# Optimization experiments

Hardware: AMD Instinct MI355X
Metric: run time of the kernel (lower is better)

Reference implementation:

```python
import jax, jax.numpy as jnp
import numpy as np

N_NODES = 50000
E_EDGES = 800000
NODE_DIM = 64
HID = 128


def _leaky(x):
    return jnp.where(x > 0, x, 0.2 * x)


def _gat_conv(x, W, a_src, a_dst, b, src, dst, heads, out_ch, concat):
    # x: [N, in]; W: [in, heads*out]; a_src/a_dst: [heads, out]
    N = x.shape[0]
    h = (x @ W).reshape(N, heads, out_ch)            # [N, H, C]
    s = (h * a_src[None]).sum(-1)                    # [N, H]
    d = (h * a_dst[None]).sum(-1)                    # [N, H]
    e = _leaky(s[src] + d[dst])                      # [E, H]
    m = jax.ops.segment_max(e, dst, num_segments=N)  # segment softmax (stable)
    ex = jnp.exp(e - m[dst])
    denom = jax.ops.segment_sum(ex, dst, num_segments=N)
    alpha = ex / denom[dst]                          # [E, H] (self-loops -> denom>0)
    out = jax.ops.segment_sum(h[src] * alpha[..., None], dst, num_segments=N)
    out = out.reshape(N, heads * out_ch) if concat else out.mean(axis=1)
    return out + b


def setup_inputs() -> dict:
    key = jax.random.key(0)
    ks = jax.random.split(key, 16)
    sc = 0.1
    inp = {
        "x": jax.random.normal(ks[0], (N_NODES, NODE_DIM), jnp.float32),
        "edge_index": jax.random.randint(ks[1], (2, E_EDGES), 0, N_NODES, jnp.int64),
        "fc_w": jax.random.normal(ks[2], (NODE_DIM, HID), jnp.float32) * sc,
        "fc_b": jnp.zeros((HID,), jnp.float32),
        "W1": jax.random.normal(ks[3], (HID, 2 * HID), jnp.float32) * sc,
        "asrc1": jax.random.normal(ks[4], (2, HID), jnp.float32) * sc,
        "adst1": jax.random.normal(ks[5], (2, HID), jnp.float32) * sc,
        "b1": jnp.zeros((2 * HID,), jnp.float32),
        "Wm": jax.random.normal(ks[6], (4, 2 * HID, 2 * HID), jnp.float32) * sc,
        "asrcm": jax.random.normal(ks[7], (4, 2, HID), jnp.float32) * sc,
        "adstm": jax.random.normal(ks[8], (4, 2, HID), jnp.float32) * sc,
        "bm": jnp.zeros((4, 2 * HID), jnp.float32),
        "W6": jax.random.normal(ks[9], (2 * HID, HID), jnp.float32) * sc,
        "asrc6": jax.random.normal(ks[10], (1, HID), jnp.float32) * sc,
        "adst6": jax.random.normal(ks[11], (1, HID), jnp.float32) * sc,
        "b6": jnp.zeros((HID,), jnp.float32),
    }
    return inp


def reference(x, edge_index, fc_w, fc_b, W1, asrc1, adst1, b1,
              Wm, asrcm, adstm, bm, W6, asrc6, adst6, b6):
    N = x.shape[0]
    loops = jnp.arange(N, dtype=edge_index.dtype)
    src = jnp.concatenate([edge_index[0], loops])  # add_self_loops=True (PyG default)
    dst = jnp.concatenate([edge_index[1], loops])

    out = jax.nn.relu(x @ fc_w + fc_b)
    out = _gat_conv(out, W1, asrc1, adst1, b1, src, dst, 2, HID, True)
    for i in range(4):
        out = _gat_conv(out, Wm[i], asrcm[i], adstm[i], bm[i], src, dst, 2, HID, True)
    out = _gat_conv(out, W6, asrc6, adst6, b6, src, dst, 1, HID, True)
    return out
```

## Files before the change

kernel.cpp:

```cpp
#include <hip/hip_runtime.h>
#include <cstdint>
#include <cstddef>

#define NN 50000
#define EE 800000
#define ET 850000

typedef unsigned short ushort_t;
typedef unsigned int uint_t;
using frag_ab = __attribute__((ext_vector_type(8))) short;
using f32x4   = __attribute__((ext_vector_type(4))) float;
using f32x2   = __attribute__((ext_vector_type(2))) float;

__device__ inline ushort_t f2b(float x) {
  union { float f; unsigned int u; } c; c.f = x;
  unsigned int u = c.u;
  u += 0x7fffu + ((u >> 16) & 1u);
  return (ushort_t)(u >> 16);
}
__device__ inline float b2f(uint_t u) {
  union { unsigned int u; float f; } c; c.u = u << 16;
  return c.f;
}
__device__ inline f32x2 unp2(uint_t u) {
  union { uint_t u; float f; } lo, hi;
  lo.u = u << 16; hi.u = u & 0xffff0000u;
  f32x2 r; r.x = lo.f; r.y = hi.f; return r;
}

__device__ inline void gload16(const ushort_t* g, ushort_t* l) {
  __builtin_amdgcn_global_load_lds(
      (const __attribute__((address_space(1))) unsigned int*)g,
      (__attribute__((address_space(3))) unsigned int*)l, 16, 0, 0);
}

__global__ __launch_bounds__(256) void k_count(const int* __restrict__ edge,
                                               int* __restrict__ counts) {
  int e = blockIdx.x * 256 + threadIdx.x;
  if (e >= ET) return;
  int dd = (e < EE) ? edge[EE + e] : (e - EE);
  atomicAdd(&counts[dd], 1);
}

__global__ __launch_bounds__(1024) void k_scan1(const int* __restrict__ counts,
                                                int* __restrict__ scn,
                                                int* __restrict__ bsum) {
  __shared__ int tmp[1024];
  int tid = threadIdx.x;
  int idx = blockIdx.x * 1024 + tid;
  int v = (idx < NN) ? counts[idx] : 0;
  tmp[tid] = v;
  __syncthreads();
  for (int o = 1; o < 1024; o <<= 1) {
    int u = (tid >= o) ? tmp[tid - o] : 0;
    __syncthreads();
    tmp[tid] += u;
    __syncthreads();
  }
  if (idx < NN) scn[idx] = tmp[tid] - v;
  if (tid == 1023) bsum[blockIdx.x] = tmp[1023];
}

__global__ __launch_bounds__(64) void k_scan2(const int* __restrict__ bsum,
                                              int* __restrict__ boff) {
  int l = threadIdx.x;
  const int NB = (NN + 1023) / 1024;
  int v = (l < NB) ? bsum[l] : 0;
  int own = v;
  for (int o = 1; o < 64; o <<= 1) {
    int u = __shfl_up(v, o);
    if (l >= o) v += u;
  }
  if (l < NB) boff[l] = v - own;
}

__global__ __launch_bounds__(1024) void k_scan3(const int* __restrict__ scn,
                                                const int* __restrict__ boff,
                                                int* __restrict__ row_ptr,
                                                int* __restrict__ cursor) {
  int idx = blockIdx.x * 1024 + threadIdx.x;
  if (idx < NN) {
    int v = scn[idx] + boff[blockIdx.x];
    row_ptr[idx] = v;
    cursor[idx] = v;
  }
  if (idx == 0) row_ptr[NN] = ET;
}

__global__ __launch_bounds__(256) void k_fill(const int* __restrict__ edge,
                                              int* __restrict__ cursor,
                                              int* __restrict__ col_src) {
  int e = blockIdx.x * 256 + threadIdx.x;
  if (e >= ET) return;
  int ss, dd;
  if (e < EE) { ss = edge[e]; dd = edge[EE + e]; }
  else        { ss = dd = e - EE; }
  int pos = atomicAdd(&cursor[dd], 1);
  col_src[pos] = ss;
}

__global__ __launch_bounds__(256) void k_prep_w(const float* __restrict__ fc_w,
                                                const float* __restrict__ W1,
                                                const float* __restrict__ Wm,
                                                const float* __restrict__ W6,
                                                ushort_t* __restrict__ fcWt,
                                                ushort_t* __restrict__ W1t,
                                                ushort_t* __restrict__ Wmt,
                                                ushort_t* __restrict__ W6t) {
  int i = blockIdx.x * 256 + threadIdx.x;
  if (i < 128 * 64) { int n = i >> 6, k = i & 63; fcWt[i] = f2b(fc_w[k * 128 + n]); return; }
  i -= 128 * 64;
  if (i < 256 * 128) { int n = i >> 7, k = i & 127; W1t[i] = f2b(W1[k * 256 + n]); return; }
  i -= 256 * 128;
  if (i < 4 * 256 * 256) {
    int l = i >> 16, r2 = i & 65535, n = r2 >> 8, k = r2 & 255;
    Wmt[i] = f2b(Wm[(size_t)l * 65536 + k * 256 + n]); return;
  }
  i -= 4 * 256 * 256;
  if (i < 128 * 256) { int n = i >> 8, k = i & 255; W6t[i] = f2b(W6[k * 128 + n]); return; }
}

__global__ __launch_bounds__(256) void k_gemm_f32(const float* __restrict__ A,
                                                  const ushort_t* __restrict__ Bt,
                                                  ushort_t* __restrict__ C,
                                                  int M, int K, int Nc,
                                                  const float* __restrict__ bias) {
  __shared__ ushort_t As[128 * 40];
  __shared__ ushort_t Bs[128 * 40];
  int row0 = blockIdx.x * 128;
  int col0 = blockIdx.y * 128;
  int t = threadIdx.x;
  int lane = t & 63, w = t >> 6;
  int wr = w >> 1, wc = w & 1;
  int r = lane & 15, kg = lane >> 4;

  f32x4 acc[4][4];
#pragma unroll
  for (int m = 0; m < 4; ++m)
#pragma unroll
    for (int n = 0; n < 4; ++n) acc[m][n] = (f32x4){0.f, 0.f, 0.f, 0.f};

  for (int k0 = 0; k0 < K; k0 += 32) {
    __syncthreads();
#pragma unroll
    for (int rep = 0; rep < 4; ++rep) {
      int c = t + rep * 256;
      int row = c >> 3, kc = c & 7;
      int grow = row0 + row;
      if (grow < M) {
        float4 v = *(const float4*)&A[(size_t)grow * K + k0 + kc * 4];
        ushort4 u;
        u.x = f2b(v.x); u.y = f2b(v.y); u.z = f2b(v.z); u.w = f2b(v.w);
        *(ushort4*)&As[row * 40 + kc * 4] = u;
      }
    }
#pragma unroll
    for (int rep = 0; rep < 2; ++rep) {
      int c = t + rep * 256;
      int row = c >> 2, kc = c & 3;
      uint4 v = *(const uint4*)&Bt[(size_t)(col0 + row) * K + k0 + kc * 8];
      *(uint4*)&Bs[row * 40 + kc * 8] = v;
    }
    __syncthreads();

    frag_ab a[4], b[4];
#pragma unroll
    for (int m = 0; m < 4; ++m)
      a[m] = *(const frag_ab*)&As[(wr * 64 + m * 16 + r) * 40 + kg * 8];
#pragma unroll
    for (int n = 0; n < 4; ++n)
      b[n] = *(const frag_ab*)&Bs[(wc * 64 + n * 16 + r) * 40 + kg * 8];
#pragma unroll
    for (int m = 0; m < 4; ++m)
#pragma unroll
      for (int n = 0; n < 4; ++n)
        acc[m][n] = __builtin_amdgcn_mfma_f32_16x16x32_bf16(a[m], b[n], acc[m][n], 0, 0, 0);
  }

#pragma unroll
  for (int m = 0; m < 4; ++m) {
    int gr0 = row0 + wr * 64 + m * 16 + kg * 4;
#pragma unroll
    for (int q = 0; q < 4; ++q) {
      int grow = gr0 + q;
      if (grow >= M) continue;
#pragma unroll
      for (int n = 0; n < 4; ++n) {
        int gcol = col0 + wc * 64 + n * 16 + r;
        float val = acc[m][n][q] + bias[gcol];
        val = fmaxf(val, 0.f);
        C[(size_t)grow * Nc + gcol] = f2b(val);
      }
    }
  }
}

__global__ __launch_bounds__(256) void k_gemm64(const ushort_t* __restrict__ A,
                                                const ushort_t* __restrict__ Bt,
                                                ushort_t* __restrict__ C,
                                                int M, int K, int Nc,
                                                const float* __restrict__ a_src,
                                                const float* __restrict__ a_dst,
                                                float* __restrict__ sbuf,
                                                float* __restrict__ dbuf,
                                                int H) {
  __shared__ ushort_t As[128 * 64];
  __shared__ ushort_t Bs[128 * 64];
  __shared__ float sdred[128][2][2];
  int row0 = blockIdx.x * 128;
  int col0 = blockIdx.y * 128;
  int t = threadIdx.x;
  int lane = t & 63, w = t >> 6;
  int wr = w >> 1, wc = w & 1;
  int r = lane & 15, kg = lane >> 4;

  f32x4 acc[4][4];
#pragma unroll
  for (int m = 0; m < 4; ++m)
#pragma unroll
    for (int n = 0; n < 4; ++n) acc[m][n] = (f32x4){0.f, 0.f, 0.f, 0.f};

  for (int k0 = 0; k0 < K; k0 += 64) {
    __syncthreads();
#pragma unroll
    for (int i = 0; i < 4; ++i) {
      int c = w * 4 + i;
      int b = c * 1024 + lane * 16;
      int row = b >> 7;
      int ks = ((b >> 4) & 7) ^ (row & 7);
      const ushort_t* ga = A + (size_t)(row0 + row) * K + k0 + ks * 8;
      if (row0 + row < M) gload16(ga, &As[c * 512]);
      const ushort_t* gb = Bt + (size_t)(col0 + row) * K + k0 + ks * 8;
      gload16(gb, &Bs[c * 512]);
    }
    __syncthreads();

#pragma unroll
    for (int kk = 0; kk < 2; ++kk) {
      frag_ab af[4], bf[4];
#pragma unroll
      for (int m = 0; m < 4; ++m) {
        int row = wr * 64 + m * 16 + r;
        int byte = row * 128 + ((kk * 64 + kg * 16) ^ ((row & 7) << 4));
        af[m] = *(const frag_ab*)((const char*)As + byte);
      }
#pragma unroll
      for (int n = 0; n < 4; ++n) {
        int row = wc * 64 + n * 16 + r;
        int byte = row * 128 + ((kk * 64 + kg * 16) ^ ((row & 7) << 4));
        bf[n] = *(const frag_ab*)((const char*)Bs + byte);
      }
#pragma unroll
      for (int m = 0; m < 4; ++m)
#pragma unroll
        for (int n = 0; n < 4; ++n)
          acc[m][n] = __builtin_amdgcn_mfma_f32_16x16x32_bf16(af[m], bf[n], acc[m][n], 0, 0, 0);
    }
  }

  int head = blockIdx.y;
  float as_[4], ad_[4];
#pragma unroll
  for (int n = 0; n < 4; ++n) {
    int cloc = wc * 64 + n * 16 + r;
    as_[n] = a_src[head * 128 + cloc];
    ad_[n] = a_dst[head * 128 + cloc];
  }

#pragma unroll
  for (int m = 0; m < 4; ++m) {
    int gr0 = row0 + wr * 64 + m * 16 + kg * 4;
#pragma unroll
    for (int q = 0; q < 4; ++q) {
      int grow = gr0 + q;
      float ps = 0.f, pd = 0.f;
      if (grow < M) {
#pragma unroll
        for (int n = 0; n < 4; ++n) {
          int gcol = col0 + wc * 64 + n * 16 + r;
          float val = acc[m][n][q];
          ps += val * as_[n]; pd += val * ad_[n];
          C[(size_t)grow * Nc + gcol] = f2b(val);
        }
      }
#pragma unroll
      for (int o = 1; o < 16; o <<= 1) {
        ps += __shfl_xor(ps, o);
        pd += __shfl_xor(pd, o);
      }
      int row_loc = wr * 64 + m * 16 + kg * 4 + q;
      if (r == 0) { sdred[row_loc][wc][0] = ps; sdred[row_loc][wc][1] = pd; }
    }
  }
  __syncthreads();
  int row = t >> 1, which = t & 1;
  int grow = row0 + row;
  if (grow < M) {
    float v = sdred[row][0][which] + sdred[row][1][which];
    float* dst = which ? dbuf : sbuf;
    dst[(size_t)grow * H + head] = v;
  }
}

__global__ __launch_bounds__(256) void k_agg2(const ushort_t* __restrict__ h2,
                                              const float* __restrict__ s,
                                              const float* __restrict__ dv,
                                              const int* __restrict__ row_ptr,
                                              const int* __restrict__ col_src,
                                              const float* __restrict__ bias,
                                              uint4* __restrict__ out) {
  int wid = threadIdx.x >> 6, l = threadIdx.x & 63;
  int n = blockIdx.x * 4 + wid;
  if (n >= NN) return;
  int beg = row_ptr[n], end = row_ptr[n + 1];
  int deg = end - beg;
  float2 tdn = ((const float2*)dv)[n];
  float dn0 = tdn.x, dn1 = tdn.y;
  int hw = l >> 5, lh = l & 31, hd = lh >> 4;
  const char* hb = (const char*)h2 + lh * 16;

  f32x2 A0 = {0.f, 0.f}, A1 = {0.f, 0.f}, A2 = {0.f, 0.f}, A3 = {0.f, 0.f};
  float d0, d1;

  if (deg <= 64) {
    int srcv = 0; float x0 = -1e30f, x1 = -1e30f;
    if (l < deg) {
      srcv = col_src[beg + l];
      float2 sv = ((const float2*)s)[srcv];
      x0 = sv.x + dn0; x0 = x0 > 0.f ? x0 : 0.2f * x0;
      x1 = sv.y + dn1; x1 = x1 > 0.f ? x1 : 0.2f * x1;
    }
    float m0 = x0, m1 = x1;
#pragma unroll
    for (int o = 1; o < 64; o <<= 1) {
      m0 = fmaxf(m0, __shfl_xor(m0, o));
      m1 = fmaxf(m1, __shfl_xor(m1, o));
    }
    float p0 = __expf(x0 - m0), p1 = __expf(x1 - m1);
    d0 = p0; d1 = p1;
#pragma unroll
    for (int o = 1; o < 64; o <<= 1) {
      d0 += __shfl_xor(d0, o);
      d1 += __shfl_xor(d1, o);
    }
    int offv = srcv << 9;
    for (int e = 0; e < deg; e += 8) {
#pragma unroll
      for (int i = 0; i < 4; ++i) {
        int ep = e + 2 * i + hw;
        int off = __shfl(offv, ep);
        float pa0 = __shfl(p0, ep);
        float pa1 = __shfl(p1, ep);
        float pa = hd ? pa1 : pa0;
        uint4 v = *(const uint4*)(hb + off);
        f32x2 pp = {pa, pa};
        A0 = __builtin_elementwise_fma(unp2(v.x), pp, A0);
        A1 = __builtin_elementwise_fma(unp2(v.y), pp, A1);
        A2 = __builtin_elementwise_fma(unp2(v.z), pp, A2);
        A3 = __builtin_elementwise_fma(unp2(v.w), pp, A3);
      }
    }
  } else {
    float m0 = -1e30f, m1 = -1e30f;
    d0 = 0.f; d1 = 0.f;
    for (int e = beg + l; e < end; e += 64) {
      int src = col_src[e];
      float2 sv = ((const float2*)s)[src];
      float x0 = sv.x + dn0; x0 = x0 > 0.f ? x0 : 0.2f * x0;
      if (x0 > m0) { d0 = d0 * __expf(m0 - x0) + 1.f; m0 = x0; } else d0 += __expf(x0 - m0);
      float x1 = sv.y + dn1; x1 = x1 > 0.f ? x1 : 0.2f * x1;
      if (x1 > m1) { d1 = d1 * __expf(m1 - x1) + 1.f; m1 = x1; } else d1 += __expf(x1 - m1);
    }
#pragma unroll
    for (int o = 1; o < 64; o <<= 1) {
      float mo = __shfl_xor(m0, o), dno = __shfl_xor(d0, o);
      float M2 = fmaxf(m0, mo);
      d0 = d0 * __expf(m0 - M2) + dno * __expf(mo - M2);
      m0 = M2;
      mo = __shfl_xor(m1, o); dno = __shfl_xor(d1, o);
      M2 = fmaxf(m1, mo);
      d1 = d1 * __expf(m1 - M2) + dno * __expf(mo - M2);
      m1 = M2;
    }
    for (int c = beg; c < end; c += 64) {
      int cnt = min(64, end - c);
      int srcv = 0; float x0 = -1e30f, x1 = -1e30f;
      if (l < cnt) {
        srcv = col_src[c + l];
        float2 sv = ((const float2*)s)[srcv];
        x0 = sv.x + dn0; x0 = x0 > 0.f ? x0 : 0.2f * x0;
        x1 = sv.y + dn1; x1 = x1 > 0.f ? x1 : 0.2f * x1;
      }
      float p0 = __expf(x0 - m0), p1 = __expf(x1 - m1);
      int offv = srcv << 9;
      for (int e = 0; e < cnt; e += 8) {
#pragma unroll
        for (int i = 0; i < 4; ++i) {
          int ep = e + 2 * i + hw;
          int off = __shfl(offv, ep);
          float pa0 = __shfl(p0, ep);
          float pa1 = __shfl(p1, ep);
          float pa = hd ? pa1 : pa0;
          uint4 v = *(const uint4*)(hb + off);
          f32x2 pp = {pa, pa};
          A0 = __builtin_elementwise_fma(unp2(v.x), pp, A0);
          A1 = __builtin_elementwise_fma(unp2(v.y), pp, A1);
          A2 = __builtin_elementwise_fma(unp2(v.z), pp, A2);
          A3 = __builtin_elementwise_fma(unp2(v.w), pp, A3);
        }
      }
    }
  }

  A0.x += __shfl_xor(A0.x, 32); A0.y += __shfl_xor(A0.y, 32);
  A1.x += __shfl_xor(A1.x, 32); A1.y += __shfl_xor(A1.y, 32);
  A2.x += __shfl_xor(A2.x, 32); A2.y += __shfl_xor(A2.y, 32);
  A3.x += __shfl_xor(A3.x, 32); A3.y += __shfl_xor(A3.y, 32);

  if (hw == 0) {
    float dh = hd ? d1 : d0;
    float inv = 1.f / dh;
    float4 b0 = ((const float4*)bias)[2 * lh];
    float4 b1 = ((const float4*)bias)[2 * lh + 1];
    uint4 ov;
    ov.x = (uint_t)f2b(A0.x * inv + b0.x) | ((uint_t)f2b(A0.y * inv + b0.y) << 16);
    ov.y = (uint_t)f2b(A1.x * inv + b0.z) | ((uint_t)f2b(A1.y * inv + b0.w) << 16);
    ov.z = (uint_t)f2b(A2.x * inv + b1.x) | ((uint_t)f2b(A2.y * inv + b1.y) << 16);
    ov.w = (uint_t)f2b(A3.x * inv + b1.z) | ((uint_t)f2b(A3.y * inv + b1.w) << 16);
    out[(size_t)n * 32 + lh] = ov;
  }
}

__global__ __launch_bounds__(256) void k_agg1(const ushort_t* __restrict__ h2,
                                              const float* __restrict__ s,
                                              const float* __restrict__ dv,
                                              const int* __restrict__ row_ptr,
                                              const int* __restrict__ col_src,
                                              const float* __restrict__ bias,
                                              float* __restrict__ out) {
  int wid = threadIdx.x >> 6, l = threadIdx.x & 63;
  int n = blockIdx.x * 4 + wid;
  if (n >= NN) return;
  int beg = row_ptr[n], end = row_ptr[n + 1];
  int deg = end - beg;
  float dn0 = dv[n];
  int hw = l >> 4, lh = l & 15;
  const char* hb = (const char*)h2 + lh * 16;

  f32x2 A0 = {0.f, 0.f}, A1 = {0.f, 0.f}, A2 = {0.f, 0.f}, A3 = {0.f, 0.f};
  float d0;

  if (deg <= 64) {
    int srcv = 0; float x0 = -1e30f;
    if (l < deg) {
      srcv = col_src[beg + l];
      x0 = s[srcv] + dn0; x0 = x0 > 0.f ? x0 : 0.2f * x0;
    }
    float m0 = x0;
#pragma unroll
    for (int o = 1; o < 64; o <<= 1) m0 = fmaxf(m0, __shfl_xor(m0, o));
    float p0 = __expf(x0 - m0);
    d0 = p0;
#pragma unroll
    for (int o = 1; o < 64; o <<= 1) d0 += __shfl_xor(d0, o);
    int offv = srcv << 8;
    for (int e = 0; e < deg; e += 8) {
#pragma unroll
      for (int i = 0; i < 2; ++i) {
        int ep = e + 4 * i + hw;
        int off = __shfl(offv, ep);
        float pa = __shfl(p0, ep);
        uint4 v = *(const uint4*)(hb + off);
        f32x2 pp = {pa, pa};
        A0 = __builtin_elementwise_fma(unp2(v.x), pp, A0);
        A1 = __builtin_elementwise_fma(unp2(v.y), pp, A1);
        A2 = __builtin_elementwise_fma(unp2(v.z), pp, A2);
        A3 = __builtin_elementwise_fma(unp2(v.w), pp, A3);
      }
    }
  } else {
    float m0 = -1e30f;
    d0 = 0.f;
    for (int e = beg + l; e < end; e += 64) {
      float x0 = s[col_src[e]] + dn0;
      x0 = x0 > 0.f ? x0 : 0.2f * x0;
      if (x0 > m0) { d0 = d0 * __expf(m0 - x0) + 1.f; m0 = x0; } else d0 += __expf(x0 - m0);
    }
#pragma unroll
    for (int o = 1; o < 64; o <<= 1) {
      float mo = __shfl_xor(m0, o), dno = __shfl_xor(d0, o);
      float M2 = fmaxf(m0, mo);
      d0 = d0 * __expf(m0 - M2) + dno * __expf(mo - M2);
      m0 = M2;
    }
    for (int c = beg; c < end; c += 64) {
      int cnt = min(64, end - c);
      int srcv = 0; float x0 = -1e30f;
      if (l < cnt) {
        srcv = col_src[c + l];
        x0 = s[srcv] + dn0; x0 = x0 > 0.f ? x0 : 0.2f * x0;
      }
      float p0 = __expf(x0 - m0);
      int offv = srcv << 8;
      for (int e = 0; e < cnt; e += 8) {
#pragma unroll
        for (int i = 0; i < 2; ++i) {
          int ep = e + 4 * i + hw;
          int off = __shfl(offv, ep);
          float pa = __shfl(p0, ep);
          uint4 v = *(const uint4*)(hb + off);
          f32x2 pp = {pa, pa};
          A0 = __builtin_elementwise_fma(unp2(v.x), pp, A0);
          A1 = __builtin_elementwise_fma(unp2(v.y), pp, A1);
          A2 = __builtin_elementwise_fma(unp2(v.z), pp, A2);
          A3 = __builtin_elementwise_fma(unp2(v.w), pp, A3);
        }
      }
    }
  }

#pragma unroll
  for (int o = 16; o < 64; o <<= 1) {
    A0.x += __shfl_xor(A0.x, o); A0.y += __shfl_xor(A0.y, o);
    A1.x += __shfl_xor(A1.x, o); A1.y += __shfl_xor(A1.y, o);
    A2.x += __shfl_xor(A2.x, o); A2.y += __shfl_xor(A2.y, o);
    A3.x += __shfl_xor(A3.x, o); A3.y += __shfl_xor(A3.y, o);
  }
  if (hw == 0) {
    float inv = 1.f / d0;
    float4 b0 = ((const float4*)bias)[2 * lh];
    float4 b1 = ((const float4*)bias)[2 * lh + 1];
    float4 o0 = make_float4(A0.x * inv + b0.x, A0.y * inv + b0.y,
                            A1.x * inv + b0.z, A1.y * inv + b0.w);
    float4 o1 = make_float4(A2.x * inv + b1.x, A2.y * inv + b1.y,
                            A3.x * inv + b1.z, A3.y * inv + b1.w);
    ((float4*)out)[(size_t)n * 32 + 2 * lh] = o0;
    ((float4*)out)[(size_t)n * 32 + 2 * lh + 1] = o1;
  }
}

extern "C" void kernel_launch(void* const* d_in, const int* in_sizes, int n_in,
                              void* d_out, int out_size, void* d_ws, size_t ws_size,
                              hipStream_t stream) {
  const float* x     = (const float*)d_in[0];
  const int*   edge  = (const int*)d_in[1];
  const float* fc_w  = (const float*)d_in[2];
  const float* fc_b  = (const float*)d_in[3];
  const float* W1    = (const float*)d_in[4];
  const float* asrc1 = (const float*)d_in[5];
  const float* adst1 = (const float*)d_in[6];
  const float* b1    = (const float*)d_in[7];
  const float* Wm    = (const float*)d_in[8];
  const float* asrcm = (const float*)d_in[9];
  const float* adstm = (const float*)d_in[10];
  const float* bm    = (const float*)d_in[11];
  const float* W6    = (const float*)d_in[12];
  const float* asrc6 = (const float*)d_in[13];
  const float* adst6 = (const float*)d_in[14];
  const float* b6    = (const float*)d_in[15];

  char* w = (char*)d_ws;
  size_t off = 0;
  auto carve = [&](size_t bytes) -> char* {
    char* p = w + off;
    off = (off + bytes + 255) & ~(size_t)255;
    return p;
  };
  ushort_t* feat0 = (ushort_t*)carve((size_t)NN * 256 * 2);
  ushort_t* feat1 = (ushort_t*)carve((size_t)NN * 256 * 2);
  ushort_t* hbuf  = (ushort_t*)carve((size_t)NN * 256 * 2);
  float* sbuf   = (float*)carve((size_t)NN * 2 * 4);
  float* dbuf   = (float*)carve((size_t)NN * 2 * 4);
  ushort_t* fcWt = (ushort_t*)carve((size_t)128 * 64 * 2);
  ushort_t* W1t  = (ushort_t*)carve((size_t)256 * 128 * 2);
  ushort_t* Wmt  = (ushort_t*)carve((size_t)4 * 256 * 256 * 2);
  ushort_t* W6t  = (ushort_t*)carve((size_t)128 * 256 * 2);
  int* counts   = (int*)carve((size_t)NN * 4);
  int* row_ptr  = (int*)carve((size_t)(NN + 1) * 4);
  int* cursor   = (int*)carve((size_t)NN * 4);
  int* col_src  = (int*)carve((size_t)ET * 4);
  int* scn      = (int*)carve((size_t)NN * 4);
  int* bsum     = (int*)carve((size_t)64 * 4);
  int* boff     = (int*)carve((size_t)64 * 4);
  (void)ws_size;

  k_prep_w<<<(335872 + 255) / 256, 256, 0, stream>>>(fc_w, W1, Wm, W6, fcWt, W1t, Wmt, W6t);

  hipMemsetAsync(counts, 0, (size_t)NN * 4, stream);
  int eb = (ET + 255) / 256;
  const int NB = (NN + 1023) / 1024;
  k_count<<<eb, 256, 0, stream>>>(edge, counts);
  k_scan1<<<NB, 1024, 0, stream>>>(counts, scn, bsum);
  k_scan2<<<1, 64, 0, stream>>>(bsum, boff);
  k_scan3<<<NB, 1024, 0, stream>>>(scn, boff, row_ptr, cursor);
  k_fill<<<eb, 256, 0, stream>>>(edge, cursor, col_src);

  dim3 g1((NN + 127) / 128, 1), g2((NN + 127) / 128, 2);
  int ab = (NN + 3) / 4;

  auto gat = [&](const ushort_t* in, int K, const ushort_t* Wt, const float* a_s,
                 const float* a_d, const float* bias, void* outp, int H) {
    k_gemm64<<<(H == 2 ? g2 : g1), 256, 0, stream>>>(
        in, Wt, hbuf, NN, K, H * 128, a_s, a_d, sbuf, dbuf, H);
    if (H == 2)
      k_agg2<<<ab, 256, 0, stream>>>(hbuf, sbuf, dbuf, row_ptr, col_src, bias, (uint4*)outp);
    else
      k_agg1<<<ab, 256, 0, stream>>>(hbuf, sbuf, dbuf, row_ptr, col_src, bias, (float*)outp);
  };

  k_gemm_f32<<<g1, 256, 0, stream>>>(x, fcWt, feat0, NN, 64, 128, fc_b);

  gat(feat0, 128, W1t, asrc1, adst1, b1, feat1, 2);

  const ushort_t* cur = feat1;
  ushort_t* nxt = feat0;
  for (int i = 0; i < 4; ++i) {
    gat(cur, 256, Wmt + (size_t)i * 256 * 256, asrcm + (size_t)i * 2 * 128,
        adstm + (size_t)i * 2 * 128, bm + (size_t)i * 256, nxt, 2);
    const ushort_t* tmp = cur;
    cur = nxt;
    nxt = (ushort_t*)tmp;
  }

  gat(cur, 256, W6t, asrc6, adst6, b6, d_out, 1);
}
```

Before: 599.7 us.

## Split GAT aggregation across feature slices per block to raise parallelism

The aggregation kernels now launch 8 (two-head) or 4 (one-head) blocks per group of nodes. Each block handles a 64-byte feature slice, and a wavefront processes 16 edges at a time with 4 lanes per slice. The first 32 neighbor rows are prefetched before the softmax reductions so the gathers overlap the shuffle chains. The cost is that the softmax max/denominator is recomputed redundantly in every slice block, and each gather is a smaller 64-byte segment, which may lower memory efficiency.

Result: slower. 1.317 ms (+119.6%).

```diff
diff --git a/kernel.cpp b/kernel.cpp
--- a/kernel.cpp
+++ b/kernel.cpp
@@ -309,50 +309,95 @@
                                               const int* __restrict__ col_src,
                                               const float* __restrict__ bias,
                                               uint4* __restrict__ out) {
+  int slice = blockIdx.x & 7;
+  int nblk = blockIdx.x >> 3;
   int wid = threadIdx.x >> 6, l = threadIdx.x & 63;
-  int n = blockIdx.x * 4 + wid;
+  int n = nblk * 4 + wid;
   if (n >= NN) return;
+  int hd = slice >> 2;
+  int sub = l & 3, eg = l >> 2;
   int beg = row_ptr[n], end = row_ptr[n + 1];
   int deg = end - beg;
-  float2 tdn = ((const float2*)dv)[n];
-  float dn0 = tdn.x, dn1 = tdn.y;
-  int hw = l >> 5, lh = l & 31, hd = lh >> 4;
-  const char* hb = (const char*)h2 + lh * 16;
+  float dnh = dv[n * 2 + hd];
+  const char* hb = (const char*)h2 + slice * 64 + sub * 16;
 
   f32x2 A0 = {0.f, 0.f}, A1 = {0.f, 0.f}, A2 = {0.f, 0.f}, A3 = {0.f, 0.f};
-  float d0, d1;
+  float den;
 
   if (deg <= 64) {
-    int srcv = 0; float x0 = -1e30f, x1 = -1e30f;
+    int srcv = 0; float x = -1e30f;
     if (l < deg) {
       srcv = col_src[beg + l];
-      float2 sv = ((const float2*)s)[srcv];
-      x0 = sv.x + dn0; x0 = x0 > 0.f ? x0 : 0.2f * x0;
-      x1 = sv.y + dn1; x1 = x1 > 0.f ? x1 : 0.2f * x1;
-    }
-    float m0 = x0, m1 = x1;
+      x = s[srcv * 2 + hd] + dnh;
+      x = x > 0.f ? x : 0.2f * x;
+    }
+    int offv = srcv << 9;
+
+    uint4 P0 = *(const uint4*)(hb + __shfl(offv, eg));
+    uint4 P1 = *(const uint4*)(hb + __shfl(offv, 16 + eg));
+
+    float m = x;
+#pragma unroll
+    for (int o = 1; o < 64; o <<= 1) m = fmaxf(m, __shfl_xor(m, o));
+    float p = __expf(x - m);
+    den = p;
+#pragma unroll
+    for (int o = 1; o < 64; o <<= 1) den += __shfl_xor(den, o);
+
+    {
+      float pa = __shfl(p, eg);
+      f32x2 pp = {pa, pa};
+      A0 = __builtin_elementwise_fma(unp2(P0.x), pp, A0);
+      A1 = __builtin_elementwise_fma(unp2(P0.y), pp, A1);
+      A2 = __builtin_elementwise_fma(unp2(P0.z), pp, A2);
+      A3 = __builtin_elementwise_fma(unp2(P0.w), pp, A3);
+      pa = __shfl(p, 16 + eg);
+      f32x2 qq = {pa, pa};
+      A0 = __builtin_elementwise_fma(unp2(P1.x), qq, A0);
+      A1 = __builtin_elementwise_fma(unp2(P1.y), qq, A1);
+      A2 = __builtin_elementwise_fma(unp2(P1.z), qq, A2);
+      A3 = __builtin_elementwise_fma(unp2(P1.w), qq, A3);
+    }
+    for (int e = 32; e < deg; e += 16) {
+      int ep = e + eg;
+      uint4 v = *(const uint4*)(hb + __shfl(offv, ep));
+      float pa = __shfl(p, ep);
+      f32x2 pp = {pa, pa};
+      A0 = __builtin_elementwise_fma(unp2(v.x), pp, A0);
+      A1 = __builtin_elementwise_fma(unp2(v.y), pp, A1);
+      A2 = __builtin_elementwise_fma(unp2(v.z), pp, A2);
+      A3 = __builtin_elementwise_fma(unp2(v.w), pp, A3);
+    }
+  } else {
+    float m = -1e30f;
+    den = 0.f;
+    for (int e = beg + l; e < end; e += 64) {
+      float x = s[col_src[e] * 2 + hd] + dnh;
+      x = x > 0.f ? x : 0.2f * x;
+      if (x > m) { den = den * __expf(m - x) + 1.f; m = x; } else den += __expf(x - m);
+    }
 #pragma unroll
     for (int o = 1; o < 64; o <<= 1) {
-      m0 = fmaxf(m0, __shfl_xor(m0, o));
-      m1 = fmaxf(m1, __shfl_xor(m1, o));
-    }
-    float p0 = __expf(x0 - m0), p1 = __expf(x1 - m1);
-    d0 = p0; d1 = p1;
-#pragma unroll
-    for (int o = 1; o < 64; o <<= 1) {
-      d0 += __shfl_xor(d0, o);
-      d1 += __shfl_xor(d1, o);
-    }
-    int offv = srcv << 9;
-    for (int e = 0; e < deg; e += 8) {
-#pragma unroll
-      for (int i = 0; i < 4; ++i) {
-        int ep = e + 2 * i + hw;
-        int off = __shfl(offv, ep);
-        float pa0 = __shfl(p0, ep);
-        float pa1 = __shfl(p1, ep);
-        float pa = hd ? pa1 : pa0;
-        uint4 v = *(const uint4*)(hb + off);
+      float mo = __shfl_xor(m, o), dno = __shfl_xor(den, o);
+      float M2 = fmaxf(m, mo);
+      den = den * __expf(m - M2) + dno * __expf(mo - M2);
+      m = M2;
+    }
+    for (int c = beg; c < end; c += 64) {
+      int cnt = min(64, end - c);
+      int srcv = 0; float x = -1e30f;
+      if (l < cnt) {
+        srcv = col_src[c + l];
+        x = s[srcv * 2 + hd] + dnh;
+        x = x > 0.f ? x : 0.2f * x;
+      }
+      float p = __expf(x - m);
+      int offv = srcv << 9;
+      for (int e = 0; e < cnt; e += 16) {
+        int ep = e + eg;
+        uint4 v = *(const uint4*)(hb + __shfl(offv, ep));
+        float pa = __shfl(p, ep);
+        if (ep >= cnt) pa = 0.f;
         f32x2 pp = {pa, pa};
         A0 = __builtin_elementwise_fma(unp2(v.x), pp, A0);
         A1 = __builtin_elementwise_fma(unp2(v.y), pp, A1);
@@ -360,74 +405,25 @@
         A3 = __builtin_elementwise_fma(unp2(v.w), pp, A3);
       }
     }
-  } else {
-    float m0 = -1e30f, m1 = -1e30f;
-    d0 = 0.f; d1 = 0.f;
-    for (int e = beg + l; e < end; e += 64) {
-      int src = col_src[e];
-      float2 sv = ((const float2*)s)[src];
-      float x0 = sv.x + dn0; x0 = x0 > 0.f ? x0 : 0.2f * x0;
-      if (x0 > m0) { d0 = d0 * __expf(m0 - x0) + 1.f; m0 = x0; } else d0 += __expf(x0 - m0);
-      float x1 = sv.y + dn1; x1 = x1 > 0.f ? x1 : 0.2f * x1;
-      if (x1 > m1) { d1 = d1 * __expf(m1 - x1) + 1.f; m1 = x1; } else d1 += __expf(x1 - m1);
-    }
-#pragma unroll
-    for (int o = 1; o < 64; o <<= 1) {
-      float mo = __shfl_xor(m0, o), dno = __shfl_xor(d0, o);
-      float M2 = fmaxf(m0, mo);
-      d0 = d0 * __expf(m0 - M2) + dno * __expf(mo - M2);
-      m0 = M2;
-      mo = __shfl_xor(m1, o); dno = __shfl_xor(d1, o);
-      M2 = fmaxf(m1, mo);
-      d1 = d1 * __expf(m1 - M2) + dno * __expf(mo - M2);
-      m1 = M2;
-    }
-    for (int c = beg; c < end; c += 64) {
-      int cnt = min(64, end - c);
-      int srcv = 0; float x0 = -1e30f, x1 = -1e30f;
-      if (l < cnt) {
-        srcv = col_src[c + l];
-        float2 sv = ((const float2*)s)[srcv];
-        x0 = sv.x + dn0; x0 = x0 > 0.f ? x0 : 0.2f * x0;
-        x1 = sv.y + dn1; x1 = x1 > 0.f ? x1 : 0.2f * x1;
-      }
-      float p0 = __expf(x0 - m0), p1 = __expf(x1 - m1);
-      int offv = srcv << 9;
-      for (int e = 0; e < cnt; e += 8) {
-#pragma unroll
-        for (int i = 0; i < 4; ++i) {
-          int ep = e + 2 * i + hw;
-          int off = __shfl(offv, ep);
-          float pa0 = __shfl(p0, ep);
-          float pa1 = __shfl(p1, ep);
-          float pa = hd ? pa1 : pa0;
-          uint4 v = *(const uint4*)(hb + off);
-          f32x2 pp = {pa, pa};
-          A0 = __builtin_elementwise_fma(unp2(v.x), pp, A0);
-          A1 = __builtin_elementwise_fma(unp2(v.y), pp, A1);
-          A2 = __builtin_elementwise_fma(unp2(v.z), pp, A2);
-          A3 = __builtin_elementwise_fma(unp2(v.w), pp, A3);
-        }
-      }
-    }
-  }
-
-  A0.x += __shfl_xor(A0.x, 32); A0.y += __shfl_xor(A0.y, 32);
-  A1.x += __shfl_xor(A1.x, 32); A1.y += __shfl_xor(A1.y, 32);
-  A2.x += __shfl_xor(A2.x, 32); A2.y += __shfl_xor(A2.y, 32);
-  A3.x += __shfl_xor(A3.x, 32); A3.y += __shfl_xor(A3.y, 32);
-
-  if (hw == 0) {
-    float dh = hd ? d1 : d0;
-    float inv = 1.f / dh;
-    float4 b0 = ((const float4*)bias)[2 * lh];
-    float4 b1 = ((const float4*)bias)[2 * lh + 1];
+  }
+
+#pragma unroll
+  for (int o = 4; o < 64; o <<= 1) {
+    A0.x += __shfl_xor(A0.x, o); A0.y += __shfl_xor(A0.y, o);
+    A1.x += __shfl_xor(A1.x, o); A1.y += __shfl_xor(A1.y, o);
+    A2.x += __shfl_xor(A2.x, o); A2.y += __shfl_xor(A2.y, o);
+    A3.x += __shfl_xor(A3.x, o); A3.y += __shfl_xor(A3.y, o);
+  }
+  if (l < 4) {
+    float inv = 1.f / den;
+    float4 b0 = ((const float4*)bias)[slice * 8 + l * 2];
+    float4 b1 = ((const float4*)bias)[slice * 8 + l * 2 + 1];
     uint4 ov;
     ov.x = (uint_t)f2b(A0.x * inv + b0.x) | ((uint_t)f2b(A0.y * inv + b0.y) << 16);
     ov.y = (uint_t)f2b(A1.x * inv + b0.z) | ((uint_t)f2b(A1.y * inv + b0.w) << 16);
     ov.z = (uint_t)f2b(A2.x * inv + b1.x) | ((uint_t)f2b(A2.y * inv + b1.y) << 16);
     ov.w = (uint_t)f2b(A3.x * inv + b1.z) | ((uint_t)f2b(A3.y * inv + b1.w) << 16);
-    out[(size_t)n * 32 + lh] = ov;
+    out[(size_t)n * 32 + slice * 4 + l] = ov;
   }
 }
 
@@ -438,39 +434,94 @@
                                               const int* __restrict__ col_src,
                                               const float* __restrict__ bias,
                                               float* __restrict__ out) {
+  int slice = blockIdx.x & 3;
+  int nblk = blockIdx.x >> 2;
   int wid = threadIdx.x >> 6, l = threadIdx.x & 63;
-  int n = blockIdx.x * 4 + wid;
+  int n = nblk * 4 + wid;
   if (n >= NN) return;
+  int sub = l & 3, eg = l >> 2;
   int beg = row_ptr[n], end = row_ptr[n + 1];
   int deg = end - beg;
   float dn0 = dv[n];
-  int hw = l >> 4, lh = l & 15;
-  const char* hb = (const char*)h2 + lh * 16;
+  const char* hb = (const char*)h2 + slice * 64 + sub * 16;
 
   f32x2 A0 = {0.f, 0.f}, A1 = {0.f, 0.f}, A2 = {0.f, 0.f}, A3 = {0.f, 0.f};
-  float d0;
+  float den;
 
   if (deg <= 64) {
-    int srcv = 0; float x0 = -1e30f;
+    int srcv = 0; float x = -1e30f;
     if (l < deg) {
       srcv = col_src[beg + l];
-      x0 = s[srcv] + dn0; x0 = x0 > 0.f ? x0 : 0.2f * x0;
-    }
-    float m0 = x0;
-#pragma unroll
-    for (int o = 1; o < 64; o <<= 1) m0 = fmaxf(m0, __shfl_xor(m0, o));
-    float p0 = __expf(x0 - m0);
-    d0 = p0;
-#pragma unroll
-    for (int o = 1; o < 64; o <<= 1) d0 += __shfl_xor(d0, o);
+      x = s[srcv] + dn0;
+      x = x > 0.f ? x : 0.2f * x;
+    }
     int offv = srcv << 8;
-    for (int e = 0; e < deg; e += 8) {
-#pragma unroll
-      for (int i = 0; i < 2; ++i) {
-        int ep = e + 4 * i + hw;
-        int off = __shfl(offv, ep);
-        float pa = __shfl(p0, ep);
-        uint4 v = *(const uint4*)(hb + off);
+
+    uint4 P0 = *(const uint4*)(hb + __shfl(offv, eg));
+    uint4 P1 = *(const uint4*)(hb + __shfl(offv, 16 + eg));
+
+    float m = x;
+#pragma unroll
+    for (int o = 1; o < 64; o <<= 1) m = fmaxf(m, __shfl_xor(m, o));
+    float p = __expf(x - m);
+    den = p;
+#pragma unroll
+    for (int o = 1; o < 64; o <<= 1) den += __shfl_xor(den, o);
+
+    {
+      float pa = __shfl(p, eg);
+      f32x2 pp = {pa, pa};
+      A0 = __builtin_elementwise_fma(unp2(P0.x), pp, A0);
+      A1 = __builtin_elementwise_fma(unp2(P0.y), pp, A1);
+      A2 = __builtin_elementwise_fma(unp2(P0.z), pp, A2);
+      A3 = __builtin_elementwise_fma(unp2(P0.w), pp, A3);
+      pa = __shfl(p, 16 + eg);
+      f32x2 qq = {pa, pa};
+      A0 = __builtin_elementwise_fma(unp2(P1.x), qq, A0);
+      A1 = __builtin_elementwise_fma(unp2(P1.y), qq, A1);
+      A2 = __builtin_elementwise_fma(unp2(P1.z), qq, A2);
+      A3 = __builtin_elementwise_fma(unp2(P1.w), qq, A3);
+    }
+    for (int e = 32; e < deg; e += 16) {
+      int ep = e + eg;
+      uint4 v = *(const uint4*)(hb + __shfl(offv, ep));
+      float pa = __shfl(p, ep);
+      f32x2 pp = {pa, pa};
+      A0 = __builtin_elementwise_fma(unp2(v.x), pp, A0);
+      A1 = __builtin_elementwise_fma(unp2(v.y), pp, A1);
+      A2 = __builtin_elementwise_fma(unp2(v.z), pp, A2);
+      A3 = __builtin_elementwise_fma(unp2(v.w), pp, A3);
+    }
+  } else {
+    float m = -1e30f;
+    den = 0.f;
+    for (int e = beg + l; e < end; e += 64) {
+      float x = s[col_src[e]] + dn0;
+      x = x > 0.f ? x : 0.2f * x;
+      if (x > m) { den = den * __expf(m - x) + 1.f; m = x; } else den += __expf(x - m);
+    }
+#pragma unroll
+    for (int o = 1; o < 64; o <<= 1) {
+      float mo = __shfl_xor(m, o), dno = __shfl_xor(den, o);
+      float M2 = fmaxf(m, mo);
+      den = den * __expf(m - M2) + dno * __expf(mo - M2);
+      m = M2;
+    }
+    for (int c = beg; c < end; c += 64) {
+      int cnt = min(64, end - c);
+      int srcv = 0; float x = -1e30f;
+      if (l < cnt) {
+        srcv = col_src[c + l];
+        x = s[srcv] + dn0;
+        x = x > 0.f ? x : 0.2f * x;
+      }
+      float p = __expf(x - m);
+      int offv = srcv << 8;
+      for (int e = 0; e < cnt; e += 16) {
+        int ep = e + eg;
+        uint4 v = *(const uint4*)(hb + __shfl(offv, ep));
+        float pa = __shfl(p, ep);
+        if (ep >= cnt) pa = 0.f;
         f32x2 pp = {pa, pa};
         A0 = __builtin_elementwise_fma(unp2(v.x), pp, A0);
         A1 = __builtin_elementwise_fma(unp2(v.y), pp, A1);
@@ -478,64 +529,25 @@
         A3 = __builtin_elementwise_fma(unp2(v.w), pp, A3);
       }
     }
-  } else {
-    float m0 = -1e30f;
-    d0 = 0.f;
-    for (int e = beg + l; e < end; e += 64) {
-      float x0 = s[col_src[e]] + dn0;
-      x0 = x0 > 0.f ? x0 : 0.2f * x0;
-      if (x0 > m0) { d0 = d0 * __expf(m0 - x0) + 1.f; m0 = x0; } else d0 += __expf(x0 - m0);
-    }
-#pragma unroll
-    for (int o = 1; o < 64; o <<= 1) {
-      float mo = __shfl_xor(m0, o), dno = __shfl_xor(d0, o);
-      float M2 = fmaxf(m0, mo);
-      d0 = d0 * __expf(m0 - M2) + dno * __expf(mo - M2);
-      m0 = M2;
-    }
-    for (int c = beg; c < end; c += 64) {
-      int cnt = min(64, end - c);
-      int srcv = 0; float x0 = -1e30f;
-      if (l < cnt) {
-        srcv = col_src[c + l];
-        x0 = s[srcv] + dn0; x0 = x0 > 0.f ? x0 : 0.2f * x0;
-      }
-      float p0 = __expf(x0 - m0);
-      int offv = srcv << 8;
-      for (int e = 0; e < cnt; e += 8) {
-#pragma unroll
-        for (int i = 0; i < 2; ++i) {
-          int ep = e + 4 * i + hw;
-          int off = __shfl(offv, ep);
-          float pa = __shfl(p0, ep);
-          uint4 v = *(const uint4*)(hb + off);
-          f32x2 pp = {pa, pa};
-          A0 = __builtin_elementwise_fma(unp2(v.x), pp, A0);
-          A1 = __builtin_elementwise_fma(unp2(v.y), pp, A1);
-          A2 = __builtin_elementwise_fma(unp2(v.z), pp, A2);
-          A3 = __builtin_elementwise_fma(unp2(v.w), pp, A3);
-        }
-      }
-    }
-  }
-
-#pragma unroll
-  for (int o = 16; o < 64; o <<= 1) {
+  }
+
+#pragma unroll
+  for (int o = 4; o < 64; o <<= 1) {
     A0.x += __shfl_xor(A0.x, o); A0.y += __shfl_xor(A0.y, o);
     A1.x += __shfl_xor(A1.x, o); A1.y += __shfl_xor(A1.y, o);
     A2.x += __shfl_xor(A2.x, o); A2.y += __shfl_xor(A2.y, o);
     A3.x += __shfl_xor(A3.x, o); A3.y += __shfl_xor(A3.y, o);
   }
-  if (hw == 0) {
-    float inv = 1.f / d0;
-    float4 b0 = ((const float4*)bias)[2 * lh];
-    float4 b1 = ((const float4*)bias)[2 * lh + 1];
+  if (l < 4) {
+    float inv = 1.f / den;
+    float4 b0 = ((const float4*)bias)[slice * 8 + l * 2];
+    float4 b1 = ((const float4*)bias)[slice * 8 + l * 2 + 1];
     float4 o0 = make_float4(A0.x * inv + b0.x, A0.y * inv + b0.y,
                             A1.x * inv + b0.z, A1.y * inv + b0.w);
     float4 o1 = make_float4(A2.x * inv + b1.x, A2.y * inv + b1.y,
                             A3.x * inv + b1.z, A3.y * inv + b1.w);
-    ((float4*)out)[(size_t)n * 32 + 2 * lh] = o0;
-    ((float4*)out)[(size_t)n * 32 + 2 * lh + 1] = o1;
+    ((float4*)out)[(size_t)n * 32 + slice * 8 + l * 2] = o0;
+    ((float4*)out)[(size_t)n * 32 + slice * 8 + l * 2 + 1] = o1;
   }
 }
 
@@ -603,9 +615,9 @@
     k_gemm64<<<(H == 2 ? g2 : g1), 256, 0, stream>>>(
         in, Wt, hbuf, NN, K, H * 128, a_s, a_d, sbuf, dbuf, H);
     if (H == 2)
-      k_agg2<<<ab, 256, 0, stream>>>(hbuf, sbuf, dbuf, row_ptr, col_src, bias, (uint4*)outp);
+      k_agg2<<<ab * 8, 256, 0, stream>>>(hbuf, sbuf, dbuf, row_ptr, col_src, bias, (uint4*)outp);
     else
-      k_agg1<<<ab, 256, 0, stream>>>(hbuf, sbuf, dbuf, row_ptr, col_src, bias, (float*)outp);
+      k_agg1<<<ab * 4, 256, 0, stream>>>(hbuf, sbuf, dbuf, row_ptr, col_src, bias, (float*)outp);
   };
 
   k_gemm_f32<<<g1, 256, 0, stream>>>(x, fcWt, feat0, NN, 64, 128, fc_b);
```
